# Optimization experiments

Measured on AMD Instinct MI355X. Metric: run time of the kernel, lower is better.

## Reference

```python
import jax, jax.numpy as jnp
import numpy as np

D_MODEL = 256
D_HEAD = 64
N_HEAD = 8


def setup_inputs() -> dict:
    key = jax.random.key(0)
    ks = jax.random.split(key, 8)
    b, h, w = 32, 64, 64
    dk = D_HEAD * N_HEAD
    s = 1.0 / np.sqrt(D_MODEL)
    x = jax.random.normal(ks[0], (b, D_MODEL, h, w), dtype=jnp.float32)
    query = jax.random.normal(ks[1], (b, D_MODEL), dtype=jnp.float32)
    Wkv = jax.random.uniform(ks[2], (2 * dk, D_MODEL), jnp.float32, -s, s)
    bkv = jax.random.uniform(ks[3], (2 * dk,), jnp.float32, -s, s)
    Wq = jax.random.uniform(ks[4], (dk, D_MODEL), jnp.float32, -s, s)
    bq = jax.random.uniform(ks[5], (dk,), jnp.float32, -s, s)
    sf = 1.0 / np.sqrt(dk)
    Wfc = jax.random.uniform(ks[6], (D_MODEL, dk), jnp.float32, -sf, sf)
    bfc = jax.random.uniform(ks[7], (D_MODEL,), jnp.float32, -sf, sf)
    return {"x": x, "query": query, "Wkv": Wkv, "bkv": bkv, "Wq": Wq, "bq": bq, "Wfc": Wfc, "bfc": bfc}


def reference(x, query, Wkv, bkv, Wq, bq, Wfc, bfc):
    b, c, h, w = x.shape
    t = h * w
    scale = 1.0 / np.sqrt(D_HEAD).astype(np.float32)
    # 1x1 conv == per-pixel linear: (b, 2*n*d, t)
    kv = jnp.einsum('bchw,oc->bohw', x, Wkv).reshape(b, 2 * N_HEAD, D_HEAD, t)
    kv = kv + bkv.reshape(1, 2 * N_HEAD, D_HEAD, 1)
    k, v = kv[:, :N_HEAD], kv[:, N_HEAD:]  # each (b, n, d, t)
    q = (query @ Wq.T + bq).reshape(b, N_HEAD, D_HEAD)
    logits = jnp.einsum('bnd,bndj->bnj', q, k) * scale
    attn = jax.nn.softmax(logits, axis=2)
    out = jnp.einsum('bnj,bndj->bnd', attn, v).reshape(b, N_HEAD * D_HEAD)
    return jax.nn.relu(out @ Wfc.T + bfc)
```

## Files before the change

kernel.cpp:

```cpp
#include <hip/hip_runtime.h>
#include <hip/hip_bf16.h>

#define B_     32
#define C_     256
#define T_     4096
#define NH_    8
#define DH_    64

__global__ __launch_bounds__(256) void k_prep(
    const float* __restrict__ query, const float* __restrict__ Wkv,
    const float* __restrict__ bkv, const float* __restrict__ Wq,
    const float* __restrict__ bq, float* __restrict__ qWt,
    float* __restrict__ qb) {
  const int n = blockIdx.x;
  const int b = blockIdx.y;
  const int t = threadIdx.x;
  __shared__ float qrow_s[C_];
  __shared__ float psum[4 * 64];
  __shared__ float qsh[64];
  __shared__ float pb_s[64];

  qrow_s[t] = query[(size_t)b * C_ + t];
  __syncthreads();

  {
    const int d = t & 63, ch = t >> 6;
    const float* wrow = Wq + (size_t)(n * DH_ + d) * C_ + ch * 64;
    const float* qr = qrow_s + ch * 64;
    float s = 0.f;
    #pragma unroll
    for (int c = 0; c < 64; c += 4) {
      float4 w = *(const float4*)(wrow + c);
      s += w.x * qr[c] + w.y * qr[c + 1] + w.z * qr[c + 2] + w.w * qr[c + 3];
    }
    psum[ch * 64 + d] = s;
  }
  __syncthreads();
  if (t < 64)
    qsh[t] = bq[n * DH_ + t] + psum[t] + psum[64 + t] + psum[128 + t] + psum[192 + t];
  __syncthreads();

  const float scale = 0.125f;
  {
    const float* wk = Wkv + (size_t)(n * DH_) * C_ + t;
    float acc = 0.f;
    #pragma unroll 8
    for (int dd = 0; dd < DH_; ++dd) acc += qsh[dd] * wk[(size_t)dd * C_];
    qWt[((size_t)b * C_ + t) * NH_ + n] = acc * scale;
  }
  if (t < 64) pb_s[t] = qsh[t] * bkv[n * DH_ + t];
  __syncthreads();
  if (t == 0) {
    float s = 0.f;
    #pragma unroll 8
    for (int dd = 0; dd < 64; ++dd) s += pb_s[dd];
    qb[b * NH_ + n] = s * scale;
  }
}

__global__ __launch_bounds__(256) void k_logits(
    const float* __restrict__ x, const float* __restrict__ qWt,
    const float* __restrict__ qbv, float* __restrict__ lgpart) {
  const int half = blockIdx.y;
  const int b = blockIdx.z;
  const int t = threadIdx.x;
  const int j = blockIdx.x * 512 + t * 2;
  __shared__ float qws[128 * NH_];

  {
    const float4 v = *(const float4*)(qWt + (size_t)b * (C_ * NH_) + half * 1024 + t * 4);
    *(float4*)(qws + t * 4) = v;
  }
  __syncthreads();

  const float* xb = x + (size_t)b * C_ * T_ + (size_t)(half * 128) * T_ + j;
  const float* qb = qbv + b * NH_;

  float acc0[NH_], acc1[NH_];
  #pragma unroll
  for (int n = 0; n < NH_; ++n) {
    const float init = half ? 0.f : qb[n];
    acc0[n] = init; acc1[n] = init;
  }

  for (int c0 = 0; c0 < 128; c0 += 8) {
    float2 xv[8];
    #pragma unroll
    for (int cc = 0; cc < 8; ++cc)
      xv[cc] = *(const float2*)(xb + (size_t)(c0 + cc) * T_);
    #pragma unroll
    for (int cc = 0; cc < 8; ++cc) {
      const float4 w0 = *(const float4*)(qws + (c0 + cc) * 8);
      const float4 w1 = *(const float4*)(qws + (c0 + cc) * 8 + 4);
      acc0[0] += w0.x * xv[cc].x; acc1[0] += w0.x * xv[cc].y;
      acc0[1] += w0.y * xv[cc].x; acc1[1] += w0.y * xv[cc].y;
      acc0[2] += w0.z * xv[cc].x; acc1[2] += w0.z * xv[cc].y;
      acc0[3] += w0.w * xv[cc].x; acc1[3] += w0.w * xv[cc].y;
      acc0[4] += w1.x * xv[cc].x; acc1[4] += w1.x * xv[cc].y;
      acc0[5] += w1.y * xv[cc].x; acc1[5] += w1.y * xv[cc].y;
      acc0[6] += w1.z * xv[cc].x; acc1[6] += w1.z * xv[cc].y;
      acc0[7] += w1.w * xv[cc].x; acc1[7] += w1.w * xv[cc].y;
    }
  }

  float* lg = lgpart + (((size_t)half * B_ + b) * NH_) * T_ + j;
  #pragma unroll
  for (int n = 0; n < NH_; ++n) {
    float2 o; o.x = acc0[n]; o.y = acc1[n];
    *(float2*)(lg + (size_t)n * T_) = o;
  }
}

__global__ __launch_bounds__(256) void k_softmax(
    const float* __restrict__ lgpart, float* __restrict__ attn) {
  const size_t row = blockIdx.x;
  const float* p0 = lgpart + row * T_;
  const float* p1 = lgpart + ((size_t)B_ * NH_ + row) * T_;
  float* pa = attn + row * T_;
  const int t = threadIdx.x;
  float4 v[4];
  #pragma unroll
  for (int i = 0; i < 4; ++i) {
    float4 a = *(const float4*)(p0 + t * 4 + i * 1024);
    float4 c = *(const float4*)(p1 + t * 4 + i * 1024);
    v[i].x = a.x + c.x; v[i].y = a.y + c.y; v[i].z = a.z + c.z; v[i].w = a.w + c.w;
  }

  float m = -3.4e38f;
  #pragma unroll
  for (int i = 0; i < 4; ++i)
    m = fmaxf(m, fmaxf(fmaxf(v[i].x, v[i].y), fmaxf(v[i].z, v[i].w)));
  #pragma unroll
  for (int o = 32; o >= 1; o >>= 1) m = fmaxf(m, __shfl_xor(m, o));
  __shared__ float sm[4];
  if ((t & 63) == 0) sm[t >> 6] = m;
  __syncthreads();
  m = fmaxf(fmaxf(sm[0], sm[1]), fmaxf(sm[2], sm[3]));

  float s = 0.f;
  #pragma unroll
  for (int i = 0; i < 4; ++i) {
    v[i].x = expf(v[i].x - m); v[i].y = expf(v[i].y - m);
    v[i].z = expf(v[i].z - m); v[i].w = expf(v[i].w - m);
    s += v[i].x + v[i].y + v[i].z + v[i].w;
  }
  #pragma unroll
  for (int o = 32; o >= 1; o >>= 1) s += __shfl_xor(s, o);
  __shared__ float ss[4];
  if ((t & 63) == 0) ss[t >> 6] = s;
  __syncthreads();
  s = ss[0] + ss[1] + ss[2] + ss[3];
  const float inv = 1.0f / s;

  #pragma unroll
  for (int i = 0; i < 4; ++i) {
    v[i].x *= inv; v[i].y *= inv; v[i].z *= inv; v[i].w *= inv;
    *(float4*)(pa + t * 4 + i * 1024) = v[i];
  }
}

#define BJ_  256
#define BJS_ 32
#define XPITCH_ 33
__global__ __launch_bounds__(256) void k_xattn(
    const float* __restrict__ x, const float* __restrict__ attn,
    float* __restrict__ part) {
  const int jt = blockIdx.x;
  const int b  = blockIdx.y;
  const int j0 = jt * BJ_;
  const int t  = threadIdx.x;
  __shared__ float xs[C_ * XPITCH_];

  const float* xb = x + (size_t)b * C_ * T_;
  const float* ab = attn + (size_t)b * NH_ * T_ + j0;

  float acc[NH_];
  #pragma unroll
  for (int n = 0; n < NH_; ++n) acc[n] = 0.f;

  const int cr = t >> 3;
  const int jc = (t & 7) * 4;

  for (int sIt = 0; sIt < BJ_ / BJS_; ++sIt) {
    const int js = sIt * BJS_;
    __syncthreads();
    #pragma unroll
    for (int p = 0; p < 8; ++p) {
      const int c = cr + p * 32;
      float4 vv = *(const float4*)(xb + (size_t)c * T_ + j0 + js + jc);
      float* dst = &xs[c * XPITCH_ + jc];
      dst[0] = vv.x; dst[1] = vv.y; dst[2] = vv.z; dst[3] = vv.w;
    }
    __syncthreads();
    const float* xr = &xs[t * XPITCH_];
    #pragma unroll 4
    for (int jj = 0; jj < BJS_; ++jj) {
      const float xv = xr[jj];
      const int j = js + jj;
      #pragma unroll
      for (int n = 0; n < NH_; ++n)
        acc[n] += ab[(size_t)n * T_ + j] * xv;
    }
  }

  float* pb = part + ((size_t)b * 16 + jt) * (NH_ * C_);
  #pragma unroll
  for (int n = 0; n < NH_; ++n) pb[n * C_ + t] = acc[n];
}

__global__ __launch_bounds__(256) void k_outv(
    const float* __restrict__ part, const float* __restrict__ Wkv,
    const float* __restrict__ bkv, float* __restrict__ outvG) {
  __shared__ float xa_s[4 * C_];
  const int hb = blockIdx.x;
  const int b  = blockIdx.y;
  const int t  = threadIdx.x;

  const float* pb = part + (size_t)b * 16 * (NH_ * C_) + hb * (4 * C_);
  #pragma unroll
  for (int r = 0; r < 4; ++r) {
    const int idx = r * 256 + t;
    float s = 0.f;
    #pragma unroll
    for (int jt = 0; jt < 16; ++jt) s += pb[(size_t)jt * (NH_ * C_) + idx];
    xa_s[idx] = s;
  }
  __syncthreads();

  const int o = hb * 256 + t;
  const float* wrow = Wkv + (size_t)(512 + o) * C_;
  const float* xa = &xa_s[(t >> 6) * C_];
  float s = bkv[512 + o];
  #pragma unroll 8
  for (int c = 0; c < C_; c += 4) {
    float4 w = *(const float4*)(wrow + c);
    s += w.x * xa[c] + w.y * xa[c + 1] + w.z * xa[c + 2] + w.w * xa[c + 3];
  }
  outvG[(size_t)b * 512 + o] = s;
}

__global__ __launch_bounds__(256) void k_fc(
    const float* __restrict__ outvG, const float* __restrict__ Wfc,
    const float* __restrict__ bfc, float* __restrict__ out) {
  __shared__ float ov[512];
  const int b = blockIdx.x;
  const int t = threadIdx.x;
  ov[t] = outvG[(size_t)b * 512 + t];
  ov[256 + t] = outvG[(size_t)b * 512 + 256 + t];
  __syncthreads();

  const float* wrow = Wfc + (size_t)t * 512;
  float s = bfc[t];
  #pragma unroll 8
  for (int o = 0; o < 512; o += 4) {
    float4 w = *(const float4*)(wrow + o);
    s += w.x * ov[o] + w.y * ov[o + 1] + w.z * ov[o + 2] + w.w * ov[o + 3];
  }
  out[(size_t)b * 256 + t] = fmaxf(s, 0.f);
}

extern "C" void kernel_launch(void* const* d_in, const int* in_sizes, int n_in,
                              void* d_out, int out_size, void* d_ws, size_t ws_size,
                              hipStream_t stream) {
  const float* x     = (const float*)d_in[0];
  const float* query = (const float*)d_in[1];
  const float* Wkv   = (const float*)d_in[2];
  const float* bkv   = (const float*)d_in[3];
  const float* Wq    = (const float*)d_in[4];
  const float* bq    = (const float*)d_in[5];
  const float* Wfc   = (const float*)d_in[6];
  const float* bfc   = (const float*)d_in[7];
  float* out = (float*)d_out;
  float* ws  = (float*)d_ws;

  float* qWt    = ws;
  float* qb     = ws + 65536;
  float* lgpart = ws + 66048;
  float* attn   = ws + 2163200;
  float* part   = ws + 3211776;
  float* outvG  = ws + 4260352;

  k_prep   <<<dim3(NH_, B_),   256, 0, stream>>>(query, Wkv, bkv, Wq, bq, qWt, qb);
  k_logits <<<dim3(8, 2, B_),  256, 0, stream>>>(x, qWt, qb, lgpart);
  k_softmax<<<B_ * NH_,        256, 0, stream>>>(lgpart, attn);
  k_xattn  <<<dim3(16, B_),    256, 0, stream>>>(x, attn, part);
  k_outv   <<<dim3(2, B_),     256, 0, stream>>>(part, Wkv, bkv, outvG);
  k_fc     <<<B_,              256, 0, stream>>>(outvG, Wfc, bfc, out);
}
```

Baseline: 273.7 us.

## Split logits over channel quarters, halve xattn tile, fuse outv and fc kernels

The logits kernel now splits the channel reduction into four quarters instead of two, doubling the grid to raise occupancy, and the softmax sums four partial logit buffers. The x·attn kernel uses 128-pixel tiles, giving twice as many blocks, and the final reduction sums 32 partials. The value projection and fc kernels are merged into one 512-thread block per batch, dropping a launch and the intermediate buffer. The cost is more partial-sum traffic through global memory and only 32 blocks for the fused tail.

```diff
diff --git a/kernel.cpp b/kernel.cpp
--- a/kernel.cpp
+++ b/kernel.cpp
@@ -61,29 +61,29 @@
 __global__ __launch_bounds__(256) void k_logits(
     const float* __restrict__ x, const float* __restrict__ qWt,
     const float* __restrict__ qbv, float* __restrict__ lgpart) {
-  const int half = blockIdx.y;
+  const int q = blockIdx.y;
   const int b = blockIdx.z;
   const int t = threadIdx.x;
   const int j = blockIdx.x * 512 + t * 2;
-  __shared__ float qws[128 * NH_];
-
-  {
-    const float4 v = *(const float4*)(qWt + (size_t)b * (C_ * NH_) + half * 1024 + t * 4);
+  __shared__ float qws[64 * NH_];
+
+  if (t < 128) {
+    const float4 v = *(const float4*)(qWt + (size_t)b * (C_ * NH_) + q * 64 * NH_ + t * 4);
     *(float4*)(qws + t * 4) = v;
   }
   __syncthreads();
 
-  const float* xb = x + (size_t)b * C_ * T_ + (size_t)(half * 128) * T_ + j;
+  const float* xb = x + ((size_t)b * C_ + q * 64) * T_ + j;
   const float* qb = qbv + b * NH_;
 
   float acc0[NH_], acc1[NH_];
   #pragma unroll
   for (int n = 0; n < NH_; ++n) {
-    const float init = half ? 0.f : qb[n];
+    const float init = (q == 0) ? qb[n] : 0.f;
     acc0[n] = init; acc1[n] = init;
   }
 
-  for (int c0 = 0; c0 < 128; c0 += 8) {
+  for (int c0 = 0; c0 < 64; c0 += 8) {
     float2 xv[8];
     #pragma unroll
     for (int cc = 0; cc < 8; ++cc)
@@ -103,7 +103,7 @@
     }
   }
 
-  float* lg = lgpart + (((size_t)half * B_ + b) * NH_) * T_ + j;
+  float* lg = lgpart + (((size_t)q * B_ + b) * NH_) * T_ + j;
   #pragma unroll
   for (int n = 0; n < NH_; ++n) {
     float2 o; o.x = acc0[n]; o.y = acc1[n];
@@ -116,14 +116,22 @@
   const size_t row = blockIdx.x;
   const float* p0 = lgpart + row * T_;
   const float* p1 = lgpart + ((size_t)B_ * NH_ + row) * T_;
+  const float* p2 = lgpart + ((size_t)2 * B_ * NH_ + row) * T_;
+  const float* p3 = lgpart + ((size_t)3 * B_ * NH_ + row) * T_;
   float* pa = attn + row * T_;
   const int t = threadIdx.x;
   float4 v[4];
   #pragma unroll
   for (int i = 0; i < 4; ++i) {
-    float4 a = *(const float4*)(p0 + t * 4 + i * 1024);
-    float4 c = *(const float4*)(p1 + t * 4 + i * 1024);
-    v[i].x = a.x + c.x; v[i].y = a.y + c.y; v[i].z = a.z + c.z; v[i].w = a.w + c.w;
+    const int off = t * 4 + i * 1024;
+    float4 a = *(const float4*)(p0 + off);
+    float4 c = *(const float4*)(p1 + off);
+    float4 d = *(const float4*)(p2 + off);
+    float4 e = *(const float4*)(p3 + off);
+    v[i].x = a.x + c.x + d.x + e.x;
+    v[i].y = a.y + c.y + d.y + e.y;
+    v[i].z = a.z + c.z + d.z + e.z;
+    v[i].w = a.w + c.w + d.w + e.w;
   }
 
   float m = -3.4e38f;
@@ -159,7 +167,7 @@
   }
 }
 
-#define BJ_  256
+#define BJ_  128
 #define BJS_ 32
 #define XPITCH_ 33
 __global__ __launch_bounds__(256) void k_xattn(
@@ -203,60 +211,55 @@
     }
   }
 
-  float* pb = part + ((size_t)b * 16 + jt) * (NH_ * C_);
+  float* pb = part + ((size_t)b * 32 + jt) * (NH_ * C_);
   #pragma unroll
   for (int n = 0; n < NH_; ++n) pb[n * C_ + t] = acc[n];
 }
 
-__global__ __launch_bounds__(256) void k_outv(
+__global__ __launch_bounds__(512) void k_out(
     const float* __restrict__ part, const float* __restrict__ Wkv,
-    const float* __restrict__ bkv, float* __restrict__ outvG) {
-  __shared__ float xa_s[4 * C_];
-  const int hb = blockIdx.x;
-  const int b  = blockIdx.y;
-  const int t  = threadIdx.x;
-
-  const float* pb = part + (size_t)b * 16 * (NH_ * C_) + hb * (4 * C_);
+    const float* __restrict__ bkv, const float* __restrict__ Wfc,
+    const float* __restrict__ bfc, float* __restrict__ out) {
+  __shared__ float xa_s[NH_ * C_];
+  __shared__ float ov_s[512];
+  const int b = blockIdx.x;
+  const int t = threadIdx.x;
+
+  const float* pb = part + (size_t)b * 32 * (NH_ * C_);
   #pragma unroll
   for (int r = 0; r < 4; ++r) {
-    const int idx = r * 256 + t;
+    const int idx = r * 512 + t;
     float s = 0.f;
     #pragma unroll
-    for (int jt = 0; jt < 16; ++jt) s += pb[(size_t)jt * (NH_ * C_) + idx];
+    for (int jt = 0; jt < 32; ++jt) s += pb[(size_t)jt * (NH_ * C_) + idx];
     xa_s[idx] = s;
   }
   __syncthreads();
 
-  const int o = hb * 256 + t;
-  const float* wrow = Wkv + (size_t)(512 + o) * C_;
-  const float* xa = &xa_s[(t >> 6) * C_];
-  float s = bkv[512 + o];
-  #pragma unroll 8
-  for (int c = 0; c < C_; c += 4) {
-    float4 w = *(const float4*)(wrow + c);
-    s += w.x * xa[c] + w.y * xa[c + 1] + w.z * xa[c + 2] + w.w * xa[c + 3];
-  }
-  outvG[(size_t)b * 512 + o] = s;
-}
-
-__global__ __launch_bounds__(256) void k_fc(
-    const float* __restrict__ outvG, const float* __restrict__ Wfc,
-    const float* __restrict__ bfc, float* __restrict__ out) {
-  __shared__ float ov[512];
-  const int b = blockIdx.x;
-  const int t = threadIdx.x;
-  ov[t] = outvG[(size_t)b * 512 + t];
-  ov[256 + t] = outvG[(size_t)b * 512 + 256 + t];
-  __syncthreads();
-
-  const float* wrow = Wfc + (size_t)t * 512;
-  float s = bfc[t];
-  #pragma unroll 8
-  for (int o = 0; o < 512; o += 4) {
-    float4 w = *(const float4*)(wrow + o);
-    s += w.x * ov[o] + w.y * ov[o + 1] + w.z * ov[o + 2] + w.w * ov[o + 3];
-  }
-  out[(size_t)b * 256 + t] = fmaxf(s, 0.f);
+  {
+    const int o = t;
+    const float* wrow = Wkv + (size_t)(512 + o) * C_;
+    const float* xa = &xa_s[(o >> 6) * C_];
+    float s = bkv[512 + o];
+    #pragma unroll 8
+    for (int c = 0; c < C_; c += 4) {
+      float4 w = *(const float4*)(wrow + c);
+      s += w.x * xa[c] + w.y * xa[c + 1] + w.z * xa[c + 2] + w.w * xa[c + 3];
+    }
+    ov_s[o] = s;
+  }
+  __syncthreads();
+
+  if (t < 256) {
+    const float* wrow = Wfc + (size_t)t * 512;
+    float s = bfc[t];
+    #pragma unroll 8
+    for (int o = 0; o < 512; o += 4) {
+      float4 w = *(const float4*)(wrow + o);
+      s += w.x * ov_s[o] + w.y * ov_s[o + 1] + w.z * ov_s[o + 2] + w.w * ov_s[o + 3];
+    }
+    out[(size_t)b * 256 + t] = fmaxf(s, 0.f);
+  }
 }
 
 extern "C" void kernel_launch(void* const* d_in, const int* in_sizes, int n_in,
@@ -276,14 +279,12 @@
   float* qWt    = ws;
   float* qb     = ws + 65536;
   float* lgpart = ws + 66048;
-  float* attn   = ws + 2163200;
-  float* part   = ws + 3211776;
-  float* outvG  = ws + 4260352;
+  float* attn   = ws + 4260352;
+  float* part   = ws + 5308928;
 
   k_prep   <<<dim3(NH_, B_),   256, 0, stream>>>(query, Wkv, bkv, Wq, bq, qWt, qb);
-  k_logits <<<dim3(8, 2, B_),  256, 0, stream>>>(x, qWt, qb, lgpart);
+  k_logits <<<dim3(8, 4, B_),  256, 0, stream>>>(x, qWt, qb, lgpart);
   k_softmax<<<B_ * NH_,        256, 0, stream>>>(lgpart, attn);
-  k_xattn  <<<dim3(16, B_),    256, 0, stream>>>(x, attn, part);
-  k_outv   <<<dim3(2, B_),     256, 0, stream>>>(part, Wkv, bkv, outvG);
-  k_fc     <<<B_,              256, 0, stream>>>(outvG, Wfc, bfc, out);
-}
+  k_xattn  <<<dim3(32, B_),    256, 0, stream>>>(x, attn, part);
+  k_out    <<<B_,              512, 0, stream>>>(part, Wkv, bkv, Wfc, bfc, out);
+}
```

Result: no change. 277.7 us (+1.5%).

## Fuse softmax into logits and xattn via per-tile max/sum statistics

Applied to the files above, without the earlier changes.

Merges the two channel halves of the logits computation into a single 512-thread block that reduces the partial sums in shared memory. Each block also emits per-tile max and sum-of-exp statistics, which removes the standalone softmax kernel along with its extra partial-logit and attention buffers. The x·attn kernel now combines those statistics and computes exp on the fly from the raw logits staged in LDS, using smaller tiles across twice as many blocks. The value-projection kernel is reorganised to launch one block per head. In exchange, the exp work is recomputed inside xattn, and there are more partial results to reduce.

```diff
diff --git a/kernel.cpp b/kernel.cpp
--- a/kernel.cpp
+++ b/kernel.cpp
@@ -58,40 +58,47 @@
   }
 }
 
-__global__ __launch_bounds__(256) void k_logits(
+__global__ __launch_bounds__(512) void k_logits(
     const float* __restrict__ x, const float* __restrict__ qWt,
-    const float* __restrict__ qbv, float* __restrict__ lgpart) {
-  const int half = blockIdx.y;
-  const int b = blockIdx.z;
-  const int t = threadIdx.x;
-  const int j = blockIdx.x * 512 + t * 2;
-  __shared__ float qws[128 * NH_];
-
-  {
-    const float4 v = *(const float4*)(qWt + (size_t)b * (C_ * NH_) + half * 1024 + t * 4);
+    const float* __restrict__ qbv, float* __restrict__ lgraw,
+    float* __restrict__ stats) {
+  const int jt = blockIdx.x;
+  const int b  = blockIdx.y;
+  const int t  = threadIdx.x;
+  const int tj = t & 255;
+  const int th = t >> 8;
+  __shared__ float qws[C_ * NH_];
+  __shared__ float red[256 * 16];
+  __shared__ float sred[8][4];
+  __shared__ float ssum[8][4];
+  __shared__ float Msh[8];
+
+  {
+    const float4 v = *(const float4*)(qWt + (size_t)b * (C_ * NH_) + t * 4);
     *(float4*)(qws + t * 4) = v;
   }
   __syncthreads();
 
-  const float* xb = x + (size_t)b * C_ * T_ + (size_t)(half * 128) * T_ + j;
+  const int j = jt * 512 + tj * 2;
+  const float* xb = x + ((size_t)b * C_ + th * 128) * T_ + j;
   const float* qb = qbv + b * NH_;
 
   float acc0[NH_], acc1[NH_];
   #pragma unroll
   for (int n = 0; n < NH_; ++n) {
-    const float init = half ? 0.f : qb[n];
+    const float init = (th == 0) ? qb[n] : 0.f;
     acc0[n] = init; acc1[n] = init;
   }
 
-  for (int c0 = 0; c0 < 128; c0 += 8) {
-    float2 xv[8];
-    #pragma unroll
-    for (int cc = 0; cc < 8; ++cc)
+  for (int c0 = 0; c0 < 128; c0 += 16) {
+    float2 xv[16];
+    #pragma unroll
+    for (int cc = 0; cc < 16; ++cc)
       xv[cc] = *(const float2*)(xb + (size_t)(c0 + cc) * T_);
     #pragma unroll
-    for (int cc = 0; cc < 8; ++cc) {
-      const float4 w0 = *(const float4*)(qws + (c0 + cc) * 8);
-      const float4 w1 = *(const float4*)(qws + (c0 + cc) * 8 + 4);
+    for (int cc = 0; cc < 16; ++cc) {
+      const float4 w0 = *(const float4*)(qws + (th * 128 + c0 + cc) * 8);
+      const float4 w1 = *(const float4*)(qws + (th * 128 + c0 + cc) * 8 + 4);
       acc0[0] += w0.x * xv[cc].x; acc1[0] += w0.x * xv[cc].y;
       acc0[1] += w0.y * xv[cc].x; acc1[1] += w0.y * xv[cc].y;
       acc0[2] += w0.z * xv[cc].x; acc1[2] += w0.z * xv[cc].y;
@@ -103,76 +110,78 @@
     }
   }
 
-  float* lg = lgpart + (((size_t)half * B_ + b) * NH_) * T_ + j;
+  if (th == 1) {
+    float* r = red + tj * 16;
+    #pragma unroll
+    for (int n = 0; n < NH_; ++n) { r[n] = acc0[n]; r[8 + n] = acc1[n]; }
+  }
+  __syncthreads();
+  if (th == 0) {
+    const float* r = red + tj * 16;
+    #pragma unroll
+    for (int n = 0; n < NH_; ++n) { acc0[n] += r[n]; acc1[n] += r[8 + n]; }
+    float* lg = lgraw + ((size_t)b * NH_) * T_ + j;
+    #pragma unroll
+    for (int n = 0; n < NH_; ++n) {
+      float2 o; o.x = acc0[n]; o.y = acc1[n];
+      *(float2*)(lg + (size_t)n * T_) = o;
+    }
+  }
+
   #pragma unroll
   for (int n = 0; n < NH_; ++n) {
-    float2 o; o.x = acc0[n]; o.y = acc1[n];
-    *(float2*)(lg + (size_t)n * T_) = o;
-  }
-}
-
-__global__ __launch_bounds__(256) void k_softmax(
-    const float* __restrict__ lgpart, float* __restrict__ attn) {
-  const size_t row = blockIdx.x;
-  const float* p0 = lgpart + row * T_;
-  const float* p1 = lgpart + ((size_t)B_ * NH_ + row) * T_;
-  float* pa = attn + row * T_;
-  const int t = threadIdx.x;
-  float4 v[4];
-  #pragma unroll
-  for (int i = 0; i < 4; ++i) {
-    float4 a = *(const float4*)(p0 + t * 4 + i * 1024);
-    float4 c = *(const float4*)(p1 + t * 4 + i * 1024);
-    v[i].x = a.x + c.x; v[i].y = a.y + c.y; v[i].z = a.z + c.z; v[i].w = a.w + c.w;
-  }
-
-  float m = -3.4e38f;
-  #pragma unroll
-  for (int i = 0; i < 4; ++i)
-    m = fmaxf(m, fmaxf(fmaxf(v[i].x, v[i].y), fmaxf(v[i].z, v[i].w)));
-  #pragma unroll
-  for (int o = 32; o >= 1; o >>= 1) m = fmaxf(m, __shfl_xor(m, o));
-  __shared__ float sm[4];
-  if ((t & 63) == 0) sm[t >> 6] = m;
-  __syncthreads();
-  m = fmaxf(fmaxf(sm[0], sm[1]), fmaxf(sm[2], sm[3]));
-
-  float s = 0.f;
-  #pragma unroll
-  for (int i = 0; i < 4; ++i) {
-    v[i].x = expf(v[i].x - m); v[i].y = expf(v[i].y - m);
-    v[i].z = expf(v[i].z - m); v[i].w = expf(v[i].w - m);
-    s += v[i].x + v[i].y + v[i].z + v[i].w;
-  }
-  #pragma unroll
-  for (int o = 32; o >= 1; o >>= 1) s += __shfl_xor(s, o);
-  __shared__ float ss[4];
-  if ((t & 63) == 0) ss[t >> 6] = s;
-  __syncthreads();
-  s = ss[0] + ss[1] + ss[2] + ss[3];
-  const float inv = 1.0f / s;
-
-  #pragma unroll
-  for (int i = 0; i < 4; ++i) {
-    v[i].x *= inv; v[i].y *= inv; v[i].z *= inv; v[i].w *= inv;
-    *(float4*)(pa + t * 4 + i * 1024) = v[i];
-  }
-}
-
-#define BJ_  256
+    float mv = fmaxf(acc0[n], acc1[n]);
+    #pragma unroll
+    for (int o = 32; o >= 1; o >>= 1) mv = fmaxf(mv, __shfl_xor(mv, o));
+    if (th == 0 && (tj & 63) == 0) sred[n][tj >> 6] = mv;
+  }
+  __syncthreads();
+  if (t < 8)
+    Msh[t] = fmaxf(fmaxf(sred[t][0], sred[t][1]), fmaxf(sred[t][2], sred[t][3]));
+  __syncthreads();
+  #pragma unroll
+  for (int n = 0; n < NH_; ++n) {
+    float sv = (th == 0) ? (expf(acc0[n] - Msh[n]) + expf(acc1[n] - Msh[n])) : 0.f;
+    #pragma unroll
+    for (int o = 32; o >= 1; o >>= 1) sv += __shfl_xor(sv, o);
+    if (th == 0 && (tj & 63) == 0) ssum[n][tj >> 6] = sv;
+  }
+  __syncthreads();
+  if (t < 8) {
+    const float S = ssum[t][0] + ssum[t][1] + ssum[t][2] + ssum[t][3];
+    float2 o; o.x = Msh[t]; o.y = S;
+    *(float2*)(stats + ((size_t)(b * NH_ + t) * 8 + jt) * 2) = o;
+  }
+}
+
+#define BJ_  128
 #define BJS_ 32
 #define XPITCH_ 33
 __global__ __launch_bounds__(256) void k_xattn(
-    const float* __restrict__ x, const float* __restrict__ attn,
-    float* __restrict__ part) {
+    const float* __restrict__ x, const float* __restrict__ lgraw,
+    const float* __restrict__ stats, float* __restrict__ part) {
   const int jt = blockIdx.x;
   const int b  = blockIdx.y;
   const int j0 = jt * BJ_;
   const int t  = threadIdx.x;
   __shared__ float xs[C_ * XPITCH_];
-
-  const float* xb = x + (size_t)b * C_ * T_;
-  const float* ab = attn + (size_t)b * NH_ * T_ + j0;
+  __shared__ float a_lds[NH_][BJS_];
+  __shared__ float Msh[NH_];
+  __shared__ float Sish[NH_];
+
+  if (t < NH_) {
+    const float* st = stats + (size_t)(b * NH_ + t) * 8 * 2;
+    float M = -3.4e38f;
+    #pragma unroll
+    for (int k = 0; k < 8; ++k) M = fmaxf(M, st[k * 2]);
+    float S = 0.f;
+    #pragma unroll
+    for (int k = 0; k < 8; ++k) S += st[k * 2 + 1] * expf(st[k * 2] - M);
+    Msh[t] = M; Sish[t] = 1.0f / S;
+  }
+
+  const float* xb  = x + (size_t)b * C_ * T_;
+  const float* lgb = lgraw + (size_t)b * NH_ * T_ + j0;
 
   float acc[NH_];
   #pragma unroll
@@ -180,6 +189,8 @@
 
   const int cr = t >> 3;
   const int jc = (t & 7) * 4;
+  const int an = t >> 5;
+  const int aj = t & 31;
 
   for (int sIt = 0; sIt < BJ_ / BJS_; ++sIt) {
     const int js = sIt * BJS_;
@@ -191,52 +202,60 @@
       float* dst = &xs[c * XPITCH_ + jc];
       dst[0] = vv.x; dst[1] = vv.y; dst[2] = vv.z; dst[3] = vv.w;
     }
+    {
+      const float lv = lgb[(size_t)an * T_ + js + aj];
+      a_lds[an][aj] = expf(lv - Msh[an]) * Sish[an];
+    }
     __syncthreads();
     const float* xr = &xs[t * XPITCH_];
     #pragma unroll 4
     for (int jj = 0; jj < BJS_; ++jj) {
       const float xv = xr[jj];
-      const int j = js + jj;
       #pragma unroll
       for (int n = 0; n < NH_; ++n)
-        acc[n] += ab[(size_t)n * T_ + j] * xv;
-    }
-  }
-
-  float* pb = part + ((size_t)b * 16 + jt) * (NH_ * C_);
+        acc[n] += a_lds[n][jj] * xv;
+    }
+  }
+
+  float* pb = part + ((size_t)b * 32 + jt) * (NH_ * C_);
   #pragma unroll
   for (int n = 0; n < NH_; ++n) pb[n * C_ + t] = acc[n];
 }
 
-__global__ __launch_bounds__(256) void k_outv(
+__global__ __launch_bounds__(256) void k_out2(
     const float* __restrict__ part, const float* __restrict__ Wkv,
     const float* __restrict__ bkv, float* __restrict__ outvG) {
-  __shared__ float xa_s[4 * C_];
-  const int hb = blockIdx.x;
-  const int b  = blockIdx.y;
-  const int t  = threadIdx.x;
-
-  const float* pb = part + (size_t)b * 16 * (NH_ * C_) + hb * (4 * C_);
-  #pragma unroll
-  for (int r = 0; r < 4; ++r) {
-    const int idx = r * 256 + t;
+  const int n = blockIdx.x;
+  const int b = blockIdx.y;
+  const int t = threadIdx.x;
+  __shared__ float xa[C_];
+  __shared__ float psum[4][64];
+
+  {
+    const float* pb = part + (size_t)b * 32 * (NH_ * C_) + n * C_ + t;
     float s = 0.f;
     #pragma unroll
-    for (int jt = 0; jt < 16; ++jt) s += pb[(size_t)jt * (NH_ * C_) + idx];
-    xa_s[idx] = s;
-  }
-  __syncthreads();
-
-  const int o = hb * 256 + t;
-  const float* wrow = Wkv + (size_t)(512 + o) * C_;
-  const float* xa = &xa_s[(t >> 6) * C_];
-  float s = bkv[512 + o];
-  #pragma unroll 8
-  for (int c = 0; c < C_; c += 4) {
-    float4 w = *(const float4*)(wrow + c);
-    s += w.x * xa[c] + w.y * xa[c + 1] + w.z * xa[c + 2] + w.w * xa[c + 3];
-  }
-  outvG[(size_t)b * 512 + o] = s;
+    for (int jt = 0; jt < 32; ++jt) s += pb[(size_t)jt * (NH_ * C_)];
+    xa[t] = s;
+  }
+  __syncthreads();
+
+  {
+    const int d = t & 63, q = t >> 6;
+    const float* wrow = Wkv + (size_t)(512 + n * 64 + d) * C_ + q * 64;
+    const float* xq = xa + q * 64;
+    float s = 0.f;
+    #pragma unroll
+    for (int c = 0; c < 64; c += 4) {
+      float4 w = *(const float4*)(wrow + c);
+      s += w.x * xq[c] + w.y * xq[c + 1] + w.z * xq[c + 2] + w.w * xq[c + 3];
+    }
+    psum[q][d] = s;
+  }
+  __syncthreads();
+  if (t < 64)
+    outvG[(size_t)b * 512 + n * 64 + t] =
+        bkv[512 + n * 64 + t] + psum[0][t] + psum[1][t] + psum[2][t] + psum[3][t];
 }
 
 __global__ __launch_bounds__(256) void k_fc(
@@ -273,17 +292,16 @@
   float* out = (float*)d_out;
   float* ws  = (float*)d_ws;
 
-  float* qWt    = ws;
-  float* qb     = ws + 65536;
-  float* lgpart = ws + 66048;
-  float* attn   = ws + 2163200;
-  float* part   = ws + 3211776;
-  float* outvG  = ws + 4260352;
-
-  k_prep   <<<dim3(NH_, B_),   256, 0, stream>>>(query, Wkv, bkv, Wq, bq, qWt, qb);
-  k_logits <<<dim3(8, 2, B_),  256, 0, stream>>>(x, qWt, qb, lgpart);
-  k_softmax<<<B_ * NH_,        256, 0, stream>>>(lgpart, attn);
-  k_xattn  <<<dim3(16, B_),    256, 0, stream>>>(x, attn, part);
-  k_outv   <<<dim3(2, B_),     256, 0, stream>>>(part, Wkv, bkv, outvG);
-  k_fc     <<<B_,              256, 0, stream>>>(outvG, Wfc, bfc, out);
-}
+  float* qWt   = ws;
+  float* qb    = ws + 65536;
+  float* stats = ws + 66048;
+  float* lgraw = ws + 70144;
+  float* part  = ws + 1118720;
+  float* outvG = ws + 3215872;
+
+  k_prep   <<<dim3(NH_, B_), 256, 0, stream>>>(query, Wkv, bkv, Wq, bq, qWt, qb);
+  k_logits <<<dim3(8, B_),   512, 0, stream>>>(x, qWt, qb, lgraw, stats);
+  k_xattn  <<<dim3(32, B_),  256, 0, stream>>>(x, lgraw, stats, part);
+  k_out2   <<<dim3(NH_, B_), 256, 0, stream>>>(part, Wkv, bkv, outvG);
+  k_fc     <<<B_,            256, 0, stream>>>(outvG, Wfc, bfc, out);
+}
```

Measured after the change: 259.6 us. -5.1%, faster.
